# Kernel tuning notes

Hardware: AMD Instinct MI355X
Metric: run time of the kernel (lower is better)

## Reference

```python
import jax, jax.numpy as jnp
import numpy as np

CHUNK = 128
EPS = 1e-6


def setup_inputs() -> dict:
    key = jax.random.key(0)
    k1, k2, k3 = jax.random.split(key, 3)
    B, H, N, D, E = 4, 8, 4096, 64, 64
    q = jax.random.uniform(k1, (B, H, N, D), dtype=jnp.float32)
    k = jax.random.uniform(k2, (B, H, N, D), dtype=jnp.float32)
    v = jax.random.normal(k3, (B, H, N, E), dtype=jnp.float32)
    return {"q": q, "k": k, "v": v, "inferrring_states": 1}


def reference(q, k, v, inferrring_states):
    # infer_hidden_states path: chunked causal linear attention with carried state.
    B, H, N, D = q.shape
    E = v.shape[-1]
    nc = N // CHUNK
    # [nc, B, H, CHUNK, *] for scan over chunks
    qc = jnp.moveaxis(q.reshape(B, H, nc, CHUNK, D), 2, 0)
    kc = jnp.moveaxis(k.reshape(B, H, nc, CHUNK, D), 2, 0)
    vc = jnp.moveaxis(v.reshape(B, H, nc, CHUNK, E), 2, 0)

    Z0 = jnp.zeros((B, H, 1, D), dtype=q.dtype)        # running sum of k
    S0 = jnp.zeros((B, H, 1, D, E), dtype=q.dtype)     # running sum of k v^T

    def step(carry, qkv):
        Z, S = carry
        qi, ki, vi = qkv
        k_cumsum = Z + jnp.cumsum(ki, axis=-2)                      # [B,H,C,D]
        D_inv = 1.0 / jnp.einsum('bhnd,bhnd->bhn', qi, k_cumsum + EPS)
        context = jnp.einsum('bhnd,bhne->bhnde', ki, vi)            # [B,H,C,D,E]
        ctx_cumsum = S + jnp.cumsum(context, axis=-3)
        out = jnp.einsum('bhnde,bhnd,bhn->bhne', ctx_cumsum, qi, D_inv)
        new_carry = (k_cumsum[:, :, -1:], ctx_cumsum[:, :, -1:])
        return new_carry, out

    (Z, S), outs = jax.lax.scan(step, (Z0, S0), (qc, kc, vc))
    out = jnp.moveaxis(outs, 0, 2).reshape(B, H, N, E)
    # states: Z=[B,H,D], S=[B,H,D,E]
    return out, Z[:, :, 0], S[:, :, 0]
```

## Files before the change

kernel.cpp:

```cpp
#include <hip/hip_runtime.h>


#define CHUNKSZ 128
#define DD 64
#define EE 64
#define NC 32
#define NBH 32
#define NSEQ 4096
#define EPSV 1e-6f
#define OUT0 (NBH * NSEQ * EE)
#define KV_ELEMS (NBH * NC * DD * EE)

typedef short bf16x8 __attribute__((ext_vector_type(8)));
typedef short bf16x4 __attribute__((ext_vector_type(4)));
typedef float f32x4  __attribute__((ext_vector_type(4)));

__device__ __forceinline__ unsigned short f2bf(float f) {
    union { float f; unsigned u; } x; x.f = f;
    unsigned u = x.u + 0x7FFFu + ((x.u >> 16) & 1u);
    return (unsigned short)(u >> 16);
}
__device__ __forceinline__ float bf2f(unsigned short s) {
    union { unsigned u; float f; } x; x.u = ((unsigned)s) << 16;
    return x.f;
}

__global__ __launch_bounds__(256) void la_phase1(
    const float* __restrict__ k, const float* __restrict__ v,
    unsigned short* __restrict__ kvT, float* __restrict__ ks)
{
    const int blk = blockIdx.x;
    const int bh = blk / NC, c = blk % NC;
    const size_t rowbase = (size_t)bh * NSEQ + (size_t)c * CHUNKSZ;

    __shared__ alignas(16) unsigned short kT[CHUNKSZ * DD];
    __shared__ alignas(16) unsigned short vT[CHUNKSZ * EE];
    __shared__ float ksp[4][DD];

    char* kb = (char*)kT;
    char* vb = (char*)vT;

    const int t = threadIdx.x;
    const int w = t >> 6, l = t & 63;
    const int lg = l >> 4, lm = l & 15;
    const int col = t & 63;

    float kpart = 0.f;
#pragma unroll
    for (int pass = 0; pass < 4; ++pass) {
        const int mg = w + 4 * pass;
        const float* kp = k + (rowbase + mg * 8) * DD + col;
        const float* vp = v + (rowbase + mg * 8) * EE + col;
        float kf[8], vf[8];
#pragma unroll
        for (int j = 0; j < 8; ++j) kf[j] = kp[(size_t)j * DD];
#pragma unroll
        for (int j = 0; j < 8; ++j) vf[j] = vp[(size_t)j * EE];
        bf16x8 ku, vu;
#pragma unroll
        for (int j = 0; j < 8; ++j) {
            kpart += kf[j];
            ku[j] = (short)f2bf(kf[j]);
            vu[j] = (short)f2bf(vf[j]);
        }
        *(bf16x8*)(kb + mg * 1024 + col * 16) = ku;
        *(bf16x8*)(vb + mg * 1024 + col * 16) = vu;
    }
    ksp[w][col] = kpart;
    __syncthreads();

    f32x4 acc[4] = {};
#pragma unroll
    for (int kk = 0; kk < 4; ++kk) {
        bf16x8 aK = *(bf16x8*)(kb + (lg + 4 * kk) * 1024 + (16 * w + lm) * 16);
#pragma unroll
        for (int ei = 0; ei < 4; ++ei) {
            bf16x8 bV = *(bf16x8*)(vb + (lg + 4 * kk) * 1024 + (16 * ei + lm) * 16);
            acc[ei] = __builtin_amdgcn_mfma_f32_16x16x32_bf16(aK, bV, acc[ei], 0, 0, 0);
        }
    }
    unsigned short* kvout = kvT + (size_t)(bh * NC + c) * DD * EE;
#pragma unroll
    for (int ei = 0; ei < 4; ++ei) {
        bf16x4 u;
        u[0] = (short)f2bf(acc[ei][0]); u[1] = (short)f2bf(acc[ei][1]);
        u[2] = (short)f2bf(acc[ei][2]); u[3] = (short)f2bf(acc[ei][3]);
        *(bf16x4*)(kvout + (16 * ei + lm) * DD + 16 * w + 4 * lg) = u;
    }
    if (t < DD)
        ks[(size_t)(bh * NC + c) * DD + t] = ksp[0][t] + ksp[1][t] + ksp[2][t] + ksp[3][t];
}

__global__ __launch_bounds__(64) void la_phase2(
    unsigned short* __restrict__ kvT, float* __restrict__ ks, float* __restrict__ out)
{
    const int bid = blockIdx.x, t = threadIdx.x;
    if (bid < 256) {
        const int gid = bid * 64 + t;
        const int bh = gid >> 9;
        const int g = gid & 511;
        unsigned short* base = kvT + (size_t)bh * (NC * DD * EE) + (size_t)g * 8;
        bf16x8 vals[NC];
#pragma unroll
        for (int c = 0; c < NC; ++c)
            vals[c] = *(const bf16x8*)(base + (size_t)c * (DD * EE));
        float run[8] = {};
#pragma unroll
        for (int c = 0; c < NC; ++c) {
            bf16x8 pr;
#pragma unroll
            for (int j = 0; j < 8; ++j) pr[j] = (short)f2bf(run[j]);
            *(bf16x8*)(base + (size_t)c * (DD * EE)) = pr;
#pragma unroll
            for (int j = 0; j < 8; ++j) run[j] += bf2f((unsigned short)vals[c][j]);
        }
        const int e = g >> 3, d0 = (g & 7) * 8;
        float* Sout = out + OUT0 + NBH * DD + (size_t)bh * DD * EE;
#pragma unroll
        for (int j = 0; j < 8; ++j)
            Sout[(size_t)(d0 + j) * EE + e] = run[j];
    } else {
        const int tid = (bid - 256) * 64 + t;
        const int bh = tid >> 6, d = tid & 63;
        float vals[NC];
#pragma unroll
        for (int c = 0; c < NC; ++c)
            vals[c] = ks[(size_t)(bh * NC + c) * DD + d];
        float run = 0.f;
#pragma unroll
        for (int c = 0; c < NC; ++c) {
            float x = vals[c];
            ks[(size_t)(bh * NC + c) * DD + d] = run;
            run += x;
        }
        out[OUT0 + tid] = run;
    }
}

__global__ __launch_bounds__(256) void la_phase3(
    const float* __restrict__ q, const float* __restrict__ k,
    const float* __restrict__ v, const unsigned short* __restrict__ kvT,
    const float* __restrict__ ks, float* __restrict__ out)
{
    const int blk = blockIdx.x;
    const int bh = blk / NC, c = blk % NC;
    const size_t rowbase = (size_t)bh * NSEQ + (size_t)c * CHUNKSZ;

    __shared__ alignas(16) unsigned short k_lds[CHUNKSZ * DD];
    __shared__ alignas(16) unsigned short v_lds[CHUNKSZ * EE];
    __shared__ alignas(16) unsigned short s_lds[CHUNKSZ * CHUNKSZ];
    __shared__ float dinv_lds[CHUNKSZ];
    __shared__ float zi_lds[DD];

    char* kb = (char*)k_lds;
    char* vb = (char*)v_lds;
    char* sb = (char*)s_lds;

    const int t  = threadIdx.x;
    const int w  = t >> 6;
    const int l  = t & 63;
    const int lg = l >> 4;
    const int lm = l & 15;
    const int ni_of[2] = { w, 7 - w };

    {
        const float4* kg = (const float4*)(k + rowbase * DD);
#pragma unroll
        for (int i = 0; i < 8; ++i) {
            int idx = t + i * 256;
            int m = idx >> 4, c4 = idx & 15;
            float4 f = kg[idx];
            bf16x4 u;
            u[0] = (short)f2bf(f.x); u[1] = (short)f2bf(f.y);
            u[2] = (short)f2bf(f.z); u[3] = (short)f2bf(f.w);
            int byt = m * 128 + ((c4 * 8) ^ ((m & 7) << 4));
            *(bf16x4*)(kb + byt) = u;
        }
    }
    {
        const int col = t & 63;
#pragma unroll
        for (int pass = 0; pass < 4; ++pass) {
            const int mg = (t >> 6) + 4 * pass;
            const float* vp = v + (rowbase + mg * 8) * EE + col;
            float vf[8];
#pragma unroll
            for (int j = 0; j < 8; ++j) vf[j] = vp[(size_t)j * EE];
            bf16x8 u;
#pragma unroll
            for (int j = 0; j < 8; ++j) u[j] = (short)f2bf(vf[j]);
            *(bf16x8*)(vb + mg * 1024 + col * 16) = u;
        }
    }
    const unsigned short* stc = kvT + (size_t)(bh * NC + c) * DD * EE;
    bf16x8 b_st[4][2];
#pragma unroll
    for (int ei = 0; ei < 4; ++ei)
#pragma unroll
        for (int kk = 0; kk < 2; ++kk)
            b_st[ei][kk] = *(const bf16x8*)(stc + (size_t)(16 * ei + lm) * DD + 8 * lg + 32 * kk);

    if (t < DD) zi_lds[t] = ks[(size_t)(bh * NC + c) * DD + t];

    bf16x8 a_q[2][2];
#pragma unroll
    for (int ni2 = 0; ni2 < 2; ++ni2) {
        int ni = ni_of[ni2];
        const float* qrow = q + (rowbase + 16 * ni + lm) * DD;
#pragma unroll
        for (int kk = 0; kk < 2; ++kk) {
            const float4* p = (const float4*)(qrow + 8 * lg + 32 * kk);
            float4 f0 = p[0], f1 = p[1];
            bf16x8 u;
            u[0] = (short)f2bf(f0.x); u[1] = (short)f2bf(f0.y);
            u[2] = (short)f2bf(f0.z); u[3] = (short)f2bf(f0.w);
            u[4] = (short)f2bf(f1.x); u[5] = (short)f2bf(f1.y);
            u[6] = (short)f2bf(f1.z); u[7] = (short)f2bf(f1.w);
            a_q[ni2][kk] = u;
        }
    }
    __syncthreads();

#pragma unroll
    for (int ni2 = 0; ni2 < 2; ++ni2) {
        const int ni = ni_of[ni2];
        const int n = 16 * ni + lm;
        float rsum = 0.f;
        for (int mi = 0; mi <= ni; ++mi) {
            f32x4 cc = {0.f, 0.f, 0.f, 0.f};
            const int mrow = 16 * mi + lm;
#pragma unroll
            for (int kk = 0; kk < 2; ++kk) {
                int byt = mrow * 128 + (((8 * lg + 32 * kk) * 2) ^ ((mrow & 7) << 4));
                bf16x8 ak = *(bf16x8*)(kb + byt);
                cc = __builtin_amdgcn_mfma_f32_16x16x32_bf16(ak, a_q[ni2][kk], cc, 0, 0, 0);
            }
            const int m0 = 16 * mi + 4 * lg;
            bf16x4 u;
#pragma unroll
            for (int r = 0; r < 4; ++r) {
                float val = (m0 + r <= n) ? cc[r] : 0.f;
                u[r] = (short)f2bf(val);
                rsum += val;
            }
            *(bf16x4*)(sb + n * 256 + ((m0 * 2) ^ ((n & 7) << 4))) = u;
        }
        if ((ni & 1) == 0) {
            bf16x4 z4 = {0, 0, 0, 0};
            const int m0 = 16 * (ni + 1) + 4 * lg;
            *(bf16x4*)(sb + n * 256 + ((m0 * 2) ^ ((n & 7) << 4))) = z4;
        }
        float qz = 0.f, qs = 0.f;
#pragma unroll
        for (int kk = 0; kk < 2; ++kk) {
#pragma unroll
            for (int i = 0; i < 8; ++i) {
                float qf = bf2f((unsigned short)a_q[ni2][kk][i]);
                qz += qf * zi_lds[8 * lg + 32 * kk + i];
                qs += qf;
            }
        }
        float part = rsum + qz + EPSV * qs;
        part += __shfl_xor(part, 16);
        part += __shfl_xor(part, 32);
        if (lg == 0) dinv_lds[n] = 1.f / part;
    }
    __syncthreads();

    f32x4 acc[2][4];
#pragma unroll
    for (int ni2 = 0; ni2 < 2; ++ni2) {
        const int ni = ni_of[ni2];
        const int kmax = (ni >> 1) + 1;
#pragma unroll
        for (int ei = 0; ei < 4; ++ei) {
            f32x4 cc = {0.f, 0.f, 0.f, 0.f};
            const int e = 16 * ei + lm;
#pragma unroll
            for (int kk = 0; kk < 2; ++kk)
                cc = __builtin_amdgcn_mfma_f32_16x16x32_bf16(a_q[ni2][kk], b_st[ei][kk], cc, 0, 0, 0);
            const int n = 16 * ni + lm;
            for (int kk = 0; kk < kmax; ++kk) {
                int bytA = n * 256 + (((8 * lg + 32 * kk) * 2) ^ ((n & 7) << 4));
                bf16x8 as = *(bf16x8*)(sb + bytA);
                int bytB = (lg + 4 * kk) * 1024 + e * 16;
                bf16x8 bv = *(bf16x8*)(vb + bytB);
                cc = __builtin_amdgcn_mfma_f32_16x16x32_bf16(as, bv, cc, 0, 0, 0);
            }
            acc[ni2][ei] = cc;
        }
    }
    __syncthreads();

#pragma unroll
    for (int ni2 = 0; ni2 < 2; ++ni2) {
        const int nbase = 16 * ni_of[ni2] + 4 * lg;
#pragma unroll
        for (int ei = 0; ei < 4; ++ei) {
            const int e = 16 * ei + lm;
#pragma unroll
            for (int r = 0; r < 4; ++r) {
                int n = nbase + r;
                out[(rowbase + n) * EE + e] = acc[ni2][ei][r] * dinv_lds[n];
            }
        }
    }
}

extern "C" void kernel_launch(void* const* d_in, const int* in_sizes, int n_in,
                              void* d_out, int out_size, void* d_ws, size_t ws_size,
                              hipStream_t stream)
{
    (void)in_sizes; (void)n_in; (void)out_size; (void)ws_size;
    const float* q = (const float*)d_in[0];
    const float* k = (const float*)d_in[1];
    const float* v = (const float*)d_in[2];
    float* out = (float*)d_out;
    unsigned short* kvT = (unsigned short*)d_ws;
    float* ks = (float*)(kvT + KV_ELEMS);

    la_phase1<<<NBH * NC, 256, 0, stream>>>(k, v, kvT, ks);
    la_phase2<<<288, 64, 0, stream>>>(kvT, ks, out);
    la_phase3<<<NBH * NC, 256, 0, stream>>>(q, k, v, kvT, ks, out);
}
```

Measured before the change: 51.37 us.

## Keep causal score tile in registers via lane shuffles instead of LDS

The masked QK^T score tile is no longer staged in shared memory. Each wave repacks its MFMA output into the A-operand layout with cross-lane shuffles and uses it directly for the S·V MFMAs. The per-row normalizer is also broadcast by shuffle instead of going through LDS, which removes two block barriers and about 33KB of LDS per block and may allow higher occupancy. In exchange it adds shuffle traffic, more register pressure from the unrolled predicated loops, and a fixed 8-iteration loop with masked bodies. Q loads now happen inside the per-tile loop rather than before the first barrier.

Measured after the change: 48.78 us, median of 2. 1.05x faster.

```diff
diff --git a/kernel.cpp b/kernel.cpp
--- a/kernel.cpp
+++ b/kernel.cpp
@@ -148,20 +148,16 @@
 
     __shared__ alignas(16) unsigned short k_lds[CHUNKSZ * DD];
     __shared__ alignas(16) unsigned short v_lds[CHUNKSZ * EE];
-    __shared__ alignas(16) unsigned short s_lds[CHUNKSZ * CHUNKSZ];
-    __shared__ float dinv_lds[CHUNKSZ];
     __shared__ float zi_lds[DD];
 
     char* kb = (char*)k_lds;
     char* vb = (char*)v_lds;
-    char* sb = (char*)s_lds;
 
     const int t  = threadIdx.x;
     const int w  = t >> 6;
     const int l  = t & 63;
     const int lg = l >> 4;
     const int lm = l & 15;
-    const int ni_of[2] = { w, 7 - w };
 
     {
         const float4* kg = (const float4*)(k + rowbase * DD);
@@ -201,61 +197,79 @@
             b_st[ei][kk] = *(const bf16x8*)(stc + (size_t)(16 * ei + lm) * DD + 8 * lg + 32 * kk);
 
     if (t < DD) zi_lds[t] = ks[(size_t)(bh * NC + c) * DD + t];
-
-    bf16x8 a_q[2][2];
+    __syncthreads();
+
+    const int src1 = 32 * (lg & 1) + lm;
+    const int src2 = src1 + 16;
+    const int par  = lg >> 1;
+
 #pragma unroll
     for (int ni2 = 0; ni2 < 2; ++ni2) {
-        int ni = ni_of[ni2];
-        const float* qrow = q + (rowbase + 16 * ni + lm) * DD;
+        const int ni = ni2 ? (7 - w) : w;
+        const int n = 16 * ni + lm;
+        const int kmax = (ni >> 1) + 1;
+
+        bf16x8 aq[2];
+        {
+            const float* qrow = q + (rowbase + n) * DD;
+#pragma unroll
+            for (int kk = 0; kk < 2; ++kk) {
+                const float4* p = (const float4*)(qrow + 8 * lg + 32 * kk);
+                float4 f0 = p[0], f1 = p[1];
+                bf16x8 u;
+                u[0] = (short)f2bf(f0.x); u[1] = (short)f2bf(f0.y);
+                u[2] = (short)f2bf(f0.z); u[3] = (short)f2bf(f0.w);
+                u[4] = (short)f2bf(f1.x); u[5] = (short)f2bf(f1.y);
+                u[6] = (short)f2bf(f1.z); u[7] = (short)f2bf(f1.w);
+                aq[kk] = u;
+            }
+        }
+
+        unsigned a_s[4][4];
+#pragma unroll
+        for (int b = 0; b < 4; ++b) {
+            a_s[b][0] = 0; a_s[b][1] = 0; a_s[b][2] = 0; a_s[b][3] = 0;
+        }
+
+        float rsum = 0.f;
+#pragma unroll
+        for (int mi = 0; mi < 8; ++mi) {
+            if (mi <= ni) {
+                f32x4 cc = {0.f, 0.f, 0.f, 0.f};
+                const int mrow = 16 * mi + lm;
+#pragma unroll
+                for (int kk = 0; kk < 2; ++kk) {
+                    int byt = mrow * 128 + (((8 * lg + 32 * kk) * 2) ^ ((mrow & 7) << 4));
+                    bf16x8 ak = *(bf16x8*)(kb + byt);
+                    cc = __builtin_amdgcn_mfma_f32_16x16x32_bf16(ak, aq[kk], cc, 0, 0, 0);
+                }
+                const int m0 = 16 * mi + 4 * lg;
+                float v0 = (m0 + 0 <= n) ? cc[0] : 0.f;
+                float v1 = (m0 + 1 <= n) ? cc[1] : 0.f;
+                float v2 = (m0 + 2 <= n) ? cc[2] : 0.f;
+                float v3 = (m0 + 3 <= n) ? cc[3] : 0.f;
+                rsum += (v0 + v1) + (v2 + v3);
+                unsigned p_lo = (unsigned)f2bf(v0) | ((unsigned)f2bf(v1) << 16);
+                unsigned p_hi = (unsigned)f2bf(v2) | ((unsigned)f2bf(v3) << 16);
+                unsigned w0 = (unsigned)__shfl((int)p_lo, src1);
+                unsigned w1 = (unsigned)__shfl((int)p_hi, src1);
+                unsigned w2 = (unsigned)__shfl((int)p_lo, src2);
+                unsigned w3 = (unsigned)__shfl((int)p_hi, src2);
+                const bool take = (par == (mi & 1));
+                const int b = mi >> 1;
+                a_s[b][0] = take ? w0 : a_s[b][0];
+                a_s[b][1] = take ? w1 : a_s[b][1];
+                a_s[b][2] = take ? w2 : a_s[b][2];
+                a_s[b][3] = take ? w3 : a_s[b][3];
+            }
+        }
+
+        float qz = 0.f, qs = 0.f;
 #pragma unroll
         for (int kk = 0; kk < 2; ++kk) {
-            const float4* p = (const float4*)(qrow + 8 * lg + 32 * kk);
-            float4 f0 = p[0], f1 = p[1];
-            bf16x8 u;
-            u[0] = (short)f2bf(f0.x); u[1] = (short)f2bf(f0.y);
-            u[2] = (short)f2bf(f0.z); u[3] = (short)f2bf(f0.w);
-            u[4] = (short)f2bf(f1.x); u[5] = (short)f2bf(f1.y);
-            u[6] = (short)f2bf(f1.z); u[7] = (short)f2bf(f1.w);
-            a_q[ni2][kk] = u;
-        }
-    }
-    __syncthreads();
-
-#pragma unroll
-    for (int ni2 = 0; ni2 < 2; ++ni2) {
-        const int ni = ni_of[ni2];
-        const int n = 16 * ni + lm;
-        float rsum = 0.f;
-        for (int mi = 0; mi <= ni; ++mi) {
-            f32x4 cc = {0.f, 0.f, 0.f, 0.f};
-            const int mrow = 16 * mi + lm;
-#pragma unroll
-            for (int kk = 0; kk < 2; ++kk) {
-                int byt = mrow * 128 + (((8 * lg + 32 * kk) * 2) ^ ((mrow & 7) << 4));
-                bf16x8 ak = *(bf16x8*)(kb + byt);
-                cc = __builtin_amdgcn_mfma_f32_16x16x32_bf16(ak, a_q[ni2][kk], cc, 0, 0, 0);
-            }
-            const int m0 = 16 * mi + 4 * lg;
-            bf16x4 u;
-#pragma unroll
-            for (int r = 0; r < 4; ++r) {
-                float val = (m0 + r <= n) ? cc[r] : 0.f;
-                u[r] = (short)f2bf(val);
-                rsum += val;
-            }
-            *(bf16x4*)(sb + n * 256 + ((m0 * 2) ^ ((n & 7) << 4))) = u;
-        }
-        if ((ni & 1) == 0) {
-            bf16x4 z4 = {0, 0, 0, 0};
-            const int m0 = 16 * (ni + 1) + 4 * lg;
-            *(bf16x4*)(sb + n * 256 + ((m0 * 2) ^ ((n & 7) << 4))) = z4;
-        }
-        float qz = 0.f, qs = 0.f;
-#pragma unroll
-        for (int kk = 0; kk < 2; ++kk) {
 #pragma unroll
             for (int i = 0; i < 8; ++i) {
-                float qf = bf2f((unsigned short)a_q[ni2][kk][i]);
+                float qf = bf2f((unsigned short)aq[kk][i]);
                 qz += qf * zi_lds[8 * lg + 32 * kk + i];
                 qs += qf;
             }
@@ -263,46 +277,37 @@
         float part = rsum + qz + EPSV * qs;
         part += __shfl_xor(part, 16);
         part += __shfl_xor(part, 32);
-        if (lg == 0) dinv_lds[n] = 1.f / part;
-    }
-    __syncthreads();
-
-    f32x4 acc[2][4];
-#pragma unroll
-    for (int ni2 = 0; ni2 < 2; ++ni2) {
-        const int ni = ni_of[ni2];
-        const int kmax = (ni >> 1) + 1;
+        const float dinv = 1.f / part;
+
+        f32x4 acc[4];
 #pragma unroll
         for (int ei = 0; ei < 4; ++ei) {
             f32x4 cc = {0.f, 0.f, 0.f, 0.f};
             const int e = 16 * ei + lm;
-#pragma unroll
-            for (int kk = 0; kk < 2; ++kk)
-                cc = __builtin_amdgcn_mfma_f32_16x16x32_bf16(a_q[ni2][kk], b_st[ei][kk], cc, 0, 0, 0);
-            const int n = 16 * ni + lm;
-            for (int kk = 0; kk < kmax; ++kk) {
-                int bytA = n * 256 + (((8 * lg + 32 * kk) * 2) ^ ((n & 7) << 4));
-                bf16x8 as = *(bf16x8*)(sb + bytA);
-                int bytB = (lg + 4 * kk) * 1024 + e * 16;
-                bf16x8 bv = *(bf16x8*)(vb + bytB);
-                cc = __builtin_amdgcn_mfma_f32_16x16x32_bf16(as, bv, cc, 0, 0, 0);
+            cc = __builtin_amdgcn_mfma_f32_16x16x32_bf16(aq[0], b_st[ei][0], cc, 0, 0, 0);
+            cc = __builtin_amdgcn_mfma_f32_16x16x32_bf16(aq[1], b_st[ei][1], cc, 0, 0, 0);
+#pragma unroll
+            for (int kk = 0; kk < 4; ++kk) {
+                if (kk < kmax) {
+                    union { unsigned u[4]; bf16x8 f; } as;
+                    as.u[0] = a_s[kk][0]; as.u[1] = a_s[kk][1];
+                    as.u[2] = a_s[kk][2]; as.u[3] = a_s[kk][3];
+                    int bytB = (lg + 4 * kk) * 1024 + e * 16;
+                    bf16x8 bv = *(bf16x8*)(vb + bytB);
+                    cc = __builtin_amdgcn_mfma_f32_16x16x32_bf16(as.f, bv, cc, 0, 0, 0);
+                }
             }
-            acc[ni2][ei] = cc;
-        }
-    }
-    __syncthreads();
-
-#pragma unroll
-    for (int ni2 = 0; ni2 < 2; ++ni2) {
-        const int nbase = 16 * ni_of[ni2] + 4 * lg;
-#pragma unroll
-        for (int ei = 0; ei < 4; ++ei) {
-            const int e = 16 * ei + lm;
-#pragma unroll
-            for (int r = 0; r < 4; ++r) {
-                int n = nbase + r;
-                out[(rowbase + n) * EE + e] = acc[ni2][ei][r] * dinv_lds[n];
-            }
+            acc[ei] = cc;
+        }
+
+#pragma unroll
+        for (int r = 0; r < 4; ++r) {
+            float dr = __shfl(dinv, 4 * lg + r);
+            const int nr = 16 * ni + 4 * lg + r;
+            float* orow = out + (rowbase + nr) * EE + lm;
+#pragma unroll
+            for (int ei = 0; ei < 4; ++ei)
+                orow[16 * ei] = acc[ei][r] * dr;
         }
     }
 }
```
